# Kernel optimization log

Hardware: AMD Instinct MI355X
Metric: run time of the kernel (lower is better)

## Reference

```python
import jax, jax.numpy as jnp
import numpy as np

M = 32768   # query length (hardcoded in __init__)
N = 32768   # kv length
QB = 128    # Q_BLOCK_SIZE
KB = 128    # KV_BLOCK_SIZE


def setup_inputs() -> dict:
    key = jax.random.key(0)
    x = jax.random.normal(key, (8, 128), dtype=jnp.float32)  # only used for device in torch
    # Reproduce the registered buffer: doc 0 on [0,4096), then one doc per 2048 tokens.
    doc = np.zeros(M, dtype=np.int32)
    for i in range(4096, M, 2048):
        doc[i:i + 2048] = i // 2048
    return {"x": x, "document_id": jnp.asarray(doc)}


@jax.jit
def _block_outputs(document_id):
    q = jnp.arange(M, dtype=jnp.int32)
    kv = jnp.arange(N, dtype=jnp.int32)
    # combined_mask = causal & document (qk is all-zeros, so where/isneginf/~ reduces to this)
    causal = q[:, None] <= kv[None, :]                       # [M, N] bool
    docm = document_id[:, None] == document_id[None, :]      # [M, N] bool
    mask = causal & docm                                     # [M, N] bool
    # _convert_mask_to_block_mask: any() over QBxKB tiles (sum>0 on bool == any)
    bm = jnp.any(mask.reshape(M // QB, QB, N // KB, KB), axis=(1, 3))
    bm = bm[None, None]                                      # [1, 1, Mb, Nb]
    bi = bm.astype(jnp.int32)
    # kv side: counts and stable descending argsort along kv-block axis
    kv_num_blocks = bi.sum(axis=3).astype(jnp.int32)                       # [1,1,Mb]
    kv_indices = jnp.argsort(-bi, axis=3).astype(jnp.int32)                # stable desc of {0,1}
    # q side: counts, stable descending argsort along q-block axis, then permute(0,1,3,2)
    q_num_blocks = bi.sum(axis=2).astype(jnp.int32)                        # [1,1,Nb]
    q_indices = jnp.argsort(-bi, axis=2).astype(jnp.int32).transpose(0, 1, 3, 2)
    return kv_num_blocks, kv_indices, q_num_blocks, q_indices


def reference(x, document_id):
    kv_num_blocks, kv_indices, q_num_blocks, q_indices = _block_outputs(document_id)
    kv_bs = jnp.array([KB], dtype=jnp.int32)
    q_bs = jnp.array([QB], dtype=jnp.int32)
    return (kv_num_blocks, kv_indices, q_num_blocks, q_indices, kv_bs, q_bs)
```

## Files before the change

### kernel.cpp

```cpp
#include <hip/hip_runtime.h>


#define NBLK 256
#define TOK  128

__device__ __forceinline__ int bm_val(int qb, int kb, const int4* S,
                                      const int* __restrict__ doc) {
    if (kb < qb) return 0;
    if (kb == qb) return 1;
    int4 a = S[qb], b = S[kb];
    if (a.y < b.x || b.y < a.x) return 0;
    if (a.z && b.z) return (a.w == b.w) ? 1 : 0;
    for (int i = 0; i < TOK; ++i) {
        int dq = doc[qb * TOK + i];
        for (int j = 0; j < TOK; ++j)
            if (dq == doc[kb * TOK + j]) return 1;
    }
    return 0;
}

__global__ __launch_bounds__(256) void fused_mask_kernel(
        const int* __restrict__ doc, int* __restrict__ out) {
    const int r = blockIdx.x;
    const int t = threadIdx.x;

    __shared__ int4 S[NBLK];
    __shared__ int wsum[4];

    {
        const int4* p = (const int4*)(doc + t * TOK);
        int4 v = p[0];
        int first = v.x;
        int mn = min(min(v.x, v.y), min(v.z, v.w));
        int mx = max(max(v.x, v.y), max(v.z, v.w));
#pragma unroll
        for (int i = 1; i < TOK / 4; ++i) {
            v = p[i];
            mn = min(mn, min(min(v.x, v.y), min(v.z, v.w)));
            mx = max(mx, max(max(v.x, v.y), max(v.z, v.w)));
        }
        S[t] = make_int4(mn, mx, (mn == mx) ? 1 : 0, first);
    }
    __syncthreads();

    int* kvn = out;
    int* kvi = out + 256;
    int* qn  = out + 256 + 65536;
    int* qi  = out + 512 + 65536;

    const int lane = t & 63;
    const int wv   = t >> 6;

    {
        int v = bm_val(r, t, S, doc);
        unsigned long long m = __ballot(v != 0);
        int prew = __popcll(m & ((1ULL << lane) - 1ULL));
        int wtot = __popcll(m);
        if (lane == 0) wsum[wv] = wtot;
        __syncthreads();
        int base = 0;
        for (int i = 0; i < wv; ++i) base += wsum[i];
        int total = wsum[0] + wsum[1] + wsum[2] + wsum[3];
        int pre = base + prew;
        int rank = v ? pre : (total + (t - pre));
        kvi[r * NBLK + rank] = t;
        if (t == 0) kvn[r] = total;
        __syncthreads();
    }

    {
        int v = bm_val(t, r, S, doc);
        unsigned long long m = __ballot(v != 0);
        int prew = __popcll(m & ((1ULL << lane) - 1ULL));
        int wtot = __popcll(m);
        if (lane == 0) wsum[wv] = wtot;
        __syncthreads();
        int base = 0;
        for (int i = 0; i < wv; ++i) base += wsum[i];
        int total = wsum[0] + wsum[1] + wsum[2] + wsum[3];
        int pre = base + prew;
        int rank = v ? pre : (total + (t - pre));
        qi[r * NBLK + rank] = t;
        if (t == 0) qn[r] = total;
    }

    if (r == 0 && t == 0) {
        out[512 + 2 * 65536 + 0] = 128;
        out[512 + 2 * 65536 + 1] = 128;
    }
}

extern "C" void kernel_launch(void* const* d_in, const int* in_sizes, int n_in,
                              void* d_out, int out_size, void* d_ws, size_t ws_size,
                              hipStream_t stream) {
    const int* doc = (const int*)d_in[1];
    int* out = (int*)d_out;

    hipLaunchKernelGGL(fused_mask_kernel, dim3(NBLK), dim3(256), 0, stream,
                       doc, out);
}
```

Baseline: 60.59 us.

## Use single-wavefront blocks with register summaries and shuffles, dropping shared memory

```diff
diff --git a/kernel.cpp b/kernel.cpp
--- a/kernel.cpp
+++ b/kernel.cpp
@@ -4,13 +4,8 @@
 #define NBLK 256
 #define TOK  128
 
-__device__ __forceinline__ int bm_val(int qb, int kb, const int4* S,
-                                      const int* __restrict__ doc) {
-    if (kb < qb) return 0;
-    if (kb == qb) return 1;
-    int4 a = S[qb], b = S[kb];
-    if (a.y < b.x || b.y < a.x) return 0;
-    if (a.z && b.z) return (a.w == b.w) ? 1 : 0;
+__device__ __noinline__ int bm_fallback(int qb, int kb,
+                                        const int* __restrict__ doc) {
     for (int i = 0; i < TOK; ++i) {
         int dq = doc[qb * TOK + i];
         for (int j = 0; j < TOK; ++j)
@@ -19,72 +14,105 @@
     return 0;
 }
 
-__global__ __launch_bounds__(256) void fused_mask_kernel(
+__device__ __forceinline__ int bm_u(int qb, int kb,
+                                    int qmn, int qmx, int qun, int qf,
+                                    int kmn, int kmx, int kun, int kf,
+                                    const int* __restrict__ doc) {
+    if (kb < qb) return 0;
+    if (kb == qb) return 1;
+    if (qmx < kmn || kmx < qmn) return 0;
+    if (qun && kun) return (qf == kf) ? 1 : 0;
+    return bm_fallback(qb, kb, doc);
+}
+
+#define SUMM(B, MN, MX, UN, FS)                                              \
+    {                                                                        \
+        const int b_ = (B);                                                  \
+        int first_ = doc[b_ * TOK];                                          \
+        int last_  = doc[b_ * TOK + TOK - 1];                                \
+        if (first_ == last_) { MN = MX = first_; UN = 1; }                   \
+        else {                                                               \
+            const int4* p_ = (const int4*)(doc + b_ * TOK);                  \
+            int mn_ = first_, mx_ = first_;                                  \
+            for (int i_ = 0; i_ < TOK / 4; ++i_) {                           \
+                int4 v_ = p_[i_];                                            \
+                mn_ = min(mn_, min(min(v_.x, v_.y), min(v_.z, v_.w)));       \
+                mx_ = max(mx_, max(max(v_.x, v_.y), max(v_.z, v_.w)));       \
+            }                                                                \
+            MN = mn_; MX = mx_; UN = 0;                                      \
+        }                                                                    \
+        FS = first_;                                                         \
+    }
+
+__global__ __launch_bounds__(64) void fused_mask_kernel(
         const int* __restrict__ doc, int* __restrict__ out) {
     const int r = blockIdx.x;
-    const int t = threadIdx.x;
+    const int l = threadIdx.x;
 
-    __shared__ int4 S[NBLK];
-    __shared__ int wsum[4];
+    int mn0, mx0, un0, f0;  SUMM(l,       mn0, mx0, un0, f0);
+    int mn1, mx1, un1, f1;  SUMM(64 + l,  mn1, mx1, un1, f1);
+    int mn2, mx2, un2, f2;  SUMM(128 + l, mn2, mx2, un2, f2);
+    int mn3, mx3, un3, f3;  SUMM(192 + l, mn3, mx3, un3, f3);
 
-    {
-        const int4* p = (const int4*)(doc + t * TOK);
-        int4 v = p[0];
-        int first = v.x;
-        int mn = min(min(v.x, v.y), min(v.z, v.w));
-        int mx = max(max(v.x, v.y), max(v.z, v.w));
-#pragma unroll
-        for (int i = 1; i < TOK / 4; ++i) {
-            v = p[i];
-            mn = min(mn, min(min(v.x, v.y), min(v.z, v.w)));
-            mx = max(mx, max(max(v.x, v.y), max(v.z, v.w)));
-        }
-        S[t] = make_int4(mn, mx, (mn == mx) ? 1 : 0, first);
-    }
-    __syncthreads();
+    const int rs = r >> 6, rl = r & 63;
+    int mnr = rs == 0 ? mn0 : rs == 1 ? mn1 : rs == 2 ? mn2 : mn3;
+    int mxr = rs == 0 ? mx0 : rs == 1 ? mx1 : rs == 2 ? mx2 : mx3;
+    int unr = rs == 0 ? un0 : rs == 1 ? un1 : rs == 2 ? un2 : un3;
+    int fr  = rs == 0 ? f0  : rs == 1 ? f1  : rs == 2 ? f2  : f3;
+    mnr = __shfl(mnr, rl);
+    mxr = __shfl(mxr, rl);
+    unr = __shfl(unr, rl);
+    fr  = __shfl(fr,  rl);
 
     int* kvn = out;
     int* kvi = out + 256;
     int* qn  = out + 256 + 65536;
     int* qi  = out + 512 + 65536;
 
-    const int lane = t & 63;
-    const int wv   = t >> 6;
+    const unsigned long long below = (1ULL << l) - 1ULL;
+    const int c0 = l, c1 = 64 + l, c2 = 128 + l, c3 = 192 + l;
 
     {
-        int v = bm_val(r, t, S, doc);
-        unsigned long long m = __ballot(v != 0);
-        int prew = __popcll(m & ((1ULL << lane) - 1ULL));
-        int wtot = __popcll(m);
-        if (lane == 0) wsum[wv] = wtot;
-        __syncthreads();
-        int base = 0;
-        for (int i = 0; i < wv; ++i) base += wsum[i];
-        int total = wsum[0] + wsum[1] + wsum[2] + wsum[3];
-        int pre = base + prew;
-        int rank = v ? pre : (total + (t - pre));
-        kvi[r * NBLK + rank] = t;
-        if (t == 0) kvn[r] = total;
-        __syncthreads();
+        int v0 = bm_u(r, c0, mnr, mxr, unr, fr, mn0, mx0, un0, f0, doc);
+        int v1 = bm_u(r, c1, mnr, mxr, unr, fr, mn1, mx1, un1, f1, doc);
+        int v2 = bm_u(r, c2, mnr, mxr, unr, fr, mn2, mx2, un2, f2, doc);
+        int v3 = bm_u(r, c3, mnr, mxr, unr, fr, mn3, mx3, un3, f3, doc);
+        unsigned long long m0 = __ballot(v0 != 0), m1 = __ballot(v1 != 0);
+        unsigned long long m2 = __ballot(v2 != 0), m3 = __ballot(v3 != 0);
+        int t0 = __popcll(m0), t1 = __popcll(m1), t2 = __popcll(m2);
+        int total = t0 + t1 + t2 + __popcll(m3);
+        int p0 = __popcll(m0 & below);
+        int p1 = t0 + __popcll(m1 & below);
+        int p2 = t0 + t1 + __popcll(m2 & below);
+        int p3 = t0 + t1 + t2 + __popcll(m3 & below);
+        kvi[r * NBLK + (v0 ? p0 : total + (c0 - p0))] = c0;
+        kvi[r * NBLK + (v1 ? p1 : total + (c1 - p1))] = c1;
+        kvi[r * NBLK + (v2 ? p2 : total + (c2 - p2))] = c2;
+        kvi[r * NBLK + (v3 ? p3 : total + (c3 - p3))] = c3;
+        if (l == 0) kvn[r] = total;
     }
 
     {
-        int v = bm_val(t, r, S, doc);
-        unsigned long long m = __ballot(v != 0);
-        int prew = __popcll(m & ((1ULL << lane) - 1ULL));
-        int wtot = __popcll(m);
-        if (lane == 0) wsum[wv] = wtot;
-        __syncthreads();
-        int base = 0;
-        for (int i = 0; i < wv; ++i) base += wsum[i];
-        int total = wsum[0] + wsum[1] + wsum[2] + wsum[3];
-        int pre = base + prew;
-        int rank = v ? pre : (total + (t - pre));
-        qi[r * NBLK + rank] = t;
-        if (t == 0) qn[r] = total;
+        int v0 = bm_u(c0, r, mn0, mx0, un0, f0, mnr, mxr, unr, fr, doc);
+        int v1 = bm_u(c1, r, mn1, mx1, un1, f1, mnr, mxr, unr, fr, doc);
+        int v2 = bm_u(c2, r, mn2, mx2, un2, f2, mnr, mxr, unr, fr, doc);
+        int v3 = bm_u(c3, r, mn3, mx3, un3, f3, mnr, mxr, unr, fr, doc);
+        unsigned long long m0 = __ballot(v0 != 0), m1 = __ballot(v1 != 0);
+        unsigned long long m2 = __ballot(v2 != 0), m3 = __ballot(v3 != 0);
+        int t0 = __popcll(m0), t1 = __popcll(m1), t2 = __popcll(m2);
+        int total = t0 + t1 + t2 + __popcll(m3);
+        int p0 = __popcll(m0 & below);
+        int p1 = t0 + __popcll(m1 & below);
+        int p2 = t0 + t1 + __popcll(m2 & below);
+        int p3 = t0 + t1 + t2 + __popcll(m3 & below);
+        qi[r * NBLK + (v0 ? p0 : total + (c0 - p0))] = c0;
+        qi[r * NBLK + (v1 ? p1 : total + (c1 - p1))] = c1;
+        qi[r * NBLK + (v2 ? p2 : total + (c2 - p2))] = c2;
+        qi[r * NBLK + (v3 ? p3 : total + (c3 - p3))] = c3;
+        if (l == 0) qn[r] = total;
     }
 
-    if (r == 0 && t == 0) {
+    if (r == 0 && l == 0) {
         out[512 + 2 * 65536 + 0] = 128;
         out[512 + 2 * 65536 + 1] = 128;
     }
@@ -96,6 +124,6 @@
     const int* doc = (const int*)d_in[1];
     int* out = (int*)d_out;
 
-    hipLaunchKernelGGL(fused_mask_kernel, dim3(NBLK), dim3(256), 0, stream,
+    hipLaunchKernelGGL(fused_mask_kernel, dim3(NBLK), dim3(64), 0, stream,
                        doc, out);
 }
```

After: 58.61 us. -3.3%, faster.
